# Kernel tuning notes

Measured on AMD Instinct MI355X. Metric: run time of the kernel, lower is better.

## Reference

```python
import jax, jax.numpy as jnp
import numpy as np

HEADS, DIM_HEAD, LANDMARKS, PINV_ITERS = 8, 64, 256, 6
DIM = 512
KERNEL = 33  # residual depthwise conv kernel size (lucidrains NystromAttention default)
EPS = 1e-5   # torch LayerNorm eps


def setup_inputs() -> dict:
    key = jax.random.key(0)
    ks = jax.random.split(key, 4)
    b, n = 4, 8192  # n divisible by LANDMARKS -> no padding branch
    w = lambda k, shape: jax.random.normal(k, shape, dtype=jnp.float32) * 0.02
    return {
        "x": jax.random.normal(ks[0], (b, n, DIM), dtype=jnp.float32),
        "ln_gamma": jnp.ones((DIM,), jnp.float32),
        "ln_beta": jnp.zeros((DIM,), jnp.float32),
        "w_qkv": w(ks[1], (DIM, 3 * HEADS * DIM_HEAD)),   # to_qkv, no bias
        "w_out": w(ks[2], (HEADS * DIM_HEAD, DIM)),
        "b_out": jnp.zeros((DIM,), jnp.float32),
        "res_kernel": w(ks[3], (HEADS, 1, KERNEL, 1)),    # Conv2d(heads, heads, (33,1), groups=heads)
    }


def _moore_penrose_pinv(a, iters):
    # iterative Moore-Penrose pseudoinverse (lucidrains)
    abs_a = jnp.abs(a)
    col = abs_a.sum(-1).max()  # global max, matching torch.max(col)
    row = abs_a.sum(-2).max()
    z = jnp.swapaxes(a, -1, -2) / (col * row)
    I = jnp.eye(a.shape[-1], dtype=a.dtype)
    for _ in range(iters):
        az = a @ z
        z = 0.25 * z @ (13.0 * I - az @ (15.0 * I - az @ (7.0 * I - az)))
    return z


def reference(x, ln_gamma, ln_beta, w_qkv, w_out, b_out, res_kernel):
    b, n, d = x.shape
    h, dh, m = HEADS, DIM_HEAD, LANDMARKS
    # --- LayerNorm ---
    mu = x.mean(-1, keepdims=True)
    var = ((x - mu) ** 2).mean(-1, keepdims=True)
    xn = (x - mu) * jax.lax.rsqrt(var + EPS) * ln_gamma + ln_beta
    # --- qkv projection ---
    qkv = xn @ w_qkv                                   # (b, n, 3*h*dh)
    q, k, v = jnp.split(qkv, 3, axis=-1)
    to_heads = lambda t: t.reshape(b, n, h, dh).transpose(0, 2, 1, 3)  # (b, h, n, dh)
    q, k, v = to_heads(q), to_heads(k), to_heads(v)
    q = q * (dh ** -0.5)
    # --- landmark pooling (mean over groups of l tokens) ---
    l = n // m
    q_l = q.reshape(b, h, m, l, dh).mean(3)            # (b, h, m, dh)
    k_l = k.reshape(b, h, m, l, dh).mean(3)
    # --- three similarity matrices + softmaxes ---
    attn1 = jax.nn.softmax(jnp.einsum('bhnd,bhmd->bhnm', q, k_l), axis=-1)    # (b,h,n,m)
    attn2 = jax.nn.softmax(jnp.einsum('bhid,bhjd->bhij', q_l, k_l), axis=-1)  # (b,h,m,m)
    attn3 = jax.nn.softmax(jnp.einsum('bhmd,bhnd->bhmn', q_l, k), axis=-1)    # (b,h,m,n)
    out = (attn1 @ _moore_penrose_pinv(attn2, PINV_ITERS)) @ (attn3 @ v)      # (b,h,n,dh)
    # --- depthwise residual conv over sequence dim (groups = heads) ---
    res = jax.lax.conv_general_dilated(
        v, res_kernel, window_strides=(1, 1),
        padding=((KERNEL // 2, KERNEL // 2), (0, 0)),
        dimension_numbers=('NCHW', 'OIHW', 'NCHW'),
        feature_group_count=h)
    out = out + res
    # --- merge heads, output projection, outer residual ---
    out = out.transpose(0, 2, 1, 3).reshape(b, n, h * dh)
    att = out @ w_out + b_out
    return x + att
```

## Files before the change

### kernel.cpp

```cpp
#include <hip/hip_runtime.h>
#include <math.h>

#define NB 4
#define NSEQ 8192
#define DMODEL 512
#define NHEADS 8
#define DHEAD 64
#define NLM 256
#define LTOK 32
#define NBH 32
#define KCONV 33
#define CH3 8

typedef unsigned short bf16_t;
typedef __attribute__((ext_vector_type(8))) short bf16x8;
typedef __attribute__((ext_vector_type(4))) float f32x4;

__device__ __forceinline__ float bf2f(bf16_t u) {
  return __uint_as_float(((unsigned)u) << 16);
}
__device__ __forceinline__ bf16_t f2bf(float f) {
  unsigned u = __float_as_uint(f);
  return (bf16_t)((u + 0x7fffu + ((u >> 16) & 1u)) >> 16);
}
__device__ __forceinline__ void bfpair(unsigned u, float& lo, float& hi) {
  lo = __uint_as_float(u << 16);
  hi = __uint_as_float(u & 0xffff0000u);
}
__device__ __forceinline__ void gload16(const bf16_t* g, bf16_t* l) {
  __builtin_amdgcn_global_load_lds(
      (const __attribute__((address_space(1))) unsigned int*)g,
      (__attribute__((address_space(3))) unsigned int*)l, 16, 0, 0);
}

__global__ __launch_bounds__(256) void ln_kernel(const float* __restrict__ x,
    const float* __restrict__ gamma, const float* __restrict__ beta,
    bf16_t* __restrict__ xn) {
  int row = blockIdx.x * 4 + (threadIdx.x >> 6);
  int lane = threadIdx.x & 63;
  const float4* xr = reinterpret_cast<const float4*>(x + (size_t)row * DMODEL);
  float4 a0 = xr[lane];
  float4 a1 = xr[lane + 64];
  float s  = a0.x + a0.y + a0.z + a0.w + a1.x + a1.y + a1.z + a1.w;
  float s2 = a0.x*a0.x + a0.y*a0.y + a0.z*a0.z + a0.w*a0.w
           + a1.x*a1.x + a1.y*a1.y + a1.z*a1.z + a1.w*a1.w;
  #pragma unroll
  for (int off = 32; off; off >>= 1) {
    s  += __shfl_down(s, off);
    s2 += __shfl_down(s2, off);
  }
  s = __shfl(s, 0); s2 = __shfl(s2, 0);
  float mu = s * (1.0f / DMODEL);
  float var = s2 * (1.0f / DMODEL) - mu * mu;
  float rs = rsqrtf(var + 1e-5f);
  const float4* g4 = reinterpret_cast<const float4*>(gamma);
  const float4* b4 = reinterpret_cast<const float4*>(beta);
  float4 g0 = g4[lane], g1 = g4[lane + 64];
  float4 bb0 = b4[lane], bb1 = b4[lane + 64];
  ushort4 o0, o1;
  o0.x = f2bf((a0.x - mu) * rs * g0.x + bb0.x);
  o0.y = f2bf((a0.y - mu) * rs * g0.y + bb0.y);
  o0.z = f2bf((a0.z - mu) * rs * g0.z + bb0.z);
  o0.w = f2bf((a0.w - mu) * rs * g0.w + bb0.w);
  o1.x = f2bf((a1.x - mu) * rs * g1.x + bb1.x);
  o1.y = f2bf((a1.y - mu) * rs * g1.y + bb1.y);
  o1.z = f2bf((a1.z - mu) * rs * g1.z + bb1.z);
  o1.w = f2bf((a1.w - mu) * rs * g1.w + bb1.w);
  ushort4* o = reinterpret_cast<ushort4*>(xn + (size_t)row * DMODEL);
  o[lane] = o0; o[lane + 64] = o1;
}

__global__ void castT2_kernel(const float* __restrict__ wqkv, const float* __restrict__ wout,
                              bf16_t* __restrict__ wqkvT, bf16_t* __restrict__ woutT,
                              unsigned int* __restrict__ scal) {
  int idx = blockIdx.x * 256 + threadIdx.x;
  if (idx == 0) scal[0] = 0x3f800000u;
  if (idx == 1) scal[1] = 0u;
  if (idx < 786432) {
    int k = idx & 511, c = idx >> 9;
    float v = wqkv[(size_t)k * 1536 + c];
    if (c < 512) v *= 0.125f;
    wqkvT[idx] = f2bf(v);
  } else {
    int i = idx - 786432;
    int k = i & 511, c = i >> 9;
    woutT[i] = f2bf(wout[(size_t)k * 512 + c]);
  }
}

__global__ __launch_bounds__(256) void gemm_qkv_mfma(const bf16_t* __restrict__ A,
    const bf16_t* __restrict__ Bt, bf16_t* __restrict__ q, bf16_t* __restrict__ k,
    bf16_t* __restrict__ v) {
  __shared__ __align__(16) bf16_t As0[128 * 32];
  __shared__ __align__(16) bf16_t As1[128 * 32];
  __shared__ __align__(16) bf16_t Bs0[128 * 32];
  __shared__ __align__(16) bf16_t Bs1[128 * 32];
  int bid = blockIdx.x;
  int xcd = bid & 7;
  int idx = bid >> 3;
  int rowT = xcd * 32 + idx / 12;
  int colT = idx % 12;
  int rowB = rowT * 128, colB = colT * 128;
  int tid = threadIdx.x;
  int wave = tid >> 6, lane = tid & 63;
  int wr = (wave >> 1) * 64, wc = (wave & 1) * 64;
  int lrow = lane & 15, g = lane >> 4;
  f32x4 acc[4][4] = {};
  for (int k0 = 0; k0 < DMODEL; k0 += 64) {
    #pragma unroll
    for (int c = 0; c < 2; ++c) {
      int eb = wave * 1024 + c * 512;
      int e = eb + lane * 8;
      int r = e >> 5, cc = e & 31;
      gload16(A + (size_t)(rowB + r) * DMODEL + k0 + cc, &As0[eb]);
      gload16(A + (size_t)(rowB + r) * DMODEL + k0 + 32 + cc, &As1[eb]);
      gload16(Bt + (size_t)(colB + r) * DMODEL + k0 + cc, &Bs0[eb]);
      gload16(Bt + (size_t)(colB + r) * DMODEL + k0 + 32 + cc, &Bs1[eb]);
    }
    __syncthreads();
    #pragma unroll
    for (int ks = 0; ks < 2; ++ks) {
      const bf16_t* Ab2 = ks ? As1 : As0;
      const bf16_t* Bb2 = ks ? Bs1 : Bs0;
      bf16x8 af[4], bf[4];
      #pragma unroll
      for (int m = 0; m < 4; ++m)
        af[m] = *reinterpret_cast<const bf16x8*>(&Ab2[(wr + m * 16 + lrow) * 32 + g * 8]);
      #pragma unroll
      for (int n = 0; n < 4; ++n)
        bf[n] = *reinterpret_cast<const bf16x8*>(&Bb2[(wc + n * 16 + lrow) * 32 + g * 8]);
      #pragma unroll
      for (int m = 0; m < 4; ++m)
        #pragma unroll
        for (int n = 0; n < 4; ++n)
          acc[m][n] = __builtin_amdgcn_mfma_f32_16x16x32_bf16(af[m], bf[n], acc[m][n], 0, 0, 0);
    }
    __syncthreads();
  }
  #pragma unroll
  for (int m = 0; m < 4; ++m) {
    #pragma unroll
    for (int n = 0; n < 4; ++n) {
      int col = colB + wc + n * 16 + lrow;
      int which = col >> 9, hc = col & 511, h = hc >> 6, d = hc & 63;
      bf16_t* dst = (which == 0) ? q : (which == 1 ? k : v);
      #pragma unroll
      for (int r = 0; r < 4; ++r) {
        int row = rowB + wr + m * 16 + g * 4 + r;
        int b = row >> 13, nn = row & 8191;
        dst[((size_t)(b * NHEADS + h) * NSEQ + nn) * DHEAD + d] = f2bf(acc[m][n][r]);
      }
    }
  }
}

__global__ __launch_bounds__(256) void gemm_out_mfma(const bf16_t* __restrict__ A,
    const bf16_t* __restrict__ Bt, const float* __restrict__ bo,
    const float* __restrict__ x, float* __restrict__ y) {
  __shared__ __align__(16) bf16_t As[128 * 32];
  __shared__ __align__(16) bf16_t Bs[128 * 32];
  int rowB = blockIdx.x * 128, colB = blockIdx.y * 128;
  int tid = threadIdx.x;
  int wave = tid >> 6, lane = tid & 63;
  int wr = (wave >> 1) * 64, wc = (wave & 1) * 64;
  int lrow = lane & 15, g = lane >> 4;
  f32x4 acc[4][4] = {};
  for (int k0 = 0; k0 < DMODEL; k0 += 32) {
    #pragma unroll
    for (int c = 0; c < 2; ++c) {
      int eb = wave * 1024 + c * 512;
      int e = eb + lane * 8;
      int r = e >> 5, cc = e & 31;
      gload16(A + (size_t)(rowB + r) * DMODEL + k0 + cc, &As[eb]);
      gload16(Bt + (size_t)(colB + r) * DMODEL + k0 + cc, &Bs[eb]);
    }
    __syncthreads();
    bf16x8 af[4], bf[4];
    #pragma unroll
    for (int m = 0; m < 4; ++m)
      af[m] = *reinterpret_cast<const bf16x8*>(&As[(wr + m * 16 + lrow) * 32 + g * 8]);
    #pragma unroll
    for (int n = 0; n < 4; ++n)
      bf[n] = *reinterpret_cast<const bf16x8*>(&Bs[(wc + n * 16 + lrow) * 32 + g * 8]);
    #pragma unroll
    for (int n = 0; n < 4; ++n)
      #pragma unroll
      for (int m = 0; m < 4; ++m)
        acc[n][m] = __builtin_amdgcn_mfma_f32_16x16x32_bf16(bf[n], af[m], acc[n][m], 0, 0, 0);
    __syncthreads();
  }
  #pragma unroll
  for (int n = 0; n < 4; ++n) {
    int c0 = colB + wc + n * 16 + g * 4;
    float4 b4 = *reinterpret_cast<const float4*>(&bo[c0]);
    #pragma unroll
    for (int m = 0; m < 4; ++m) {
      int row = rowB + wr + m * 16 + lrow;
      size_t off = (size_t)row * DMODEL + c0;
      float4 xv = *reinterpret_cast<const float4*>(&x[off]);
      float4 o;
      o.x = xv.x + b4.x + acc[n][m][0];
      o.y = xv.y + b4.y + acc[n][m][1];
      o.z = xv.z + b4.z + acc[n][m][2];
      o.w = xv.w + b4.w + acc[n][m][3];
      *reinterpret_cast<float4*>(&y[off]) = o;
    }
  }
}

__global__ __launch_bounds__(256) void transpose64_kernel(const bf16_t* __restrict__ src,
    bf16_t* __restrict__ dst, int R) {
  __shared__ __align__(16) bf16_t T[64 * 64];
  int r0 = blockIdx.x * 64, bh = blockIdx.y;
  int tid = threadIdx.x;
  int jj = tid >> 2, part = tid & 3;
  const uint4* sr = reinterpret_cast<const uint4*>(
      src + ((size_t)bh * R + r0 + jj) * 64 + part * 16);
  uint4 a0 = sr[0], a1 = sr[1];
  int xr = (jj >> 3) & 7;
  int pg0 = (part * 2) ^ xr, pg1 = (part * 2 + 1) ^ xr;
  *reinterpret_cast<uint4*>(&T[jj * 64 + pg0 * 8]) = a0;
  *reinterpret_cast<uint4*>(&T[jj * 64 + pg1 * 8]) = a1;
  __syncthreads();
  int d = tid >> 2;
  unsigned ow[8];
  #pragma unroll
  for (int ee = 0; ee < 8; ++ee) {
    int n1 = part * 16 + ee * 2, n2 = n1 + 1;
    unsigned lo = T[n1 * 64 + (((d >> 3) ^ ((n1 >> 3) & 7)) * 8) + (d & 7)];
    unsigned hi = T[n2 * 64 + (((d >> 3) ^ ((n2 >> 3) & 7)) * 8) + (d & 7)];
    ow[ee] = lo | (hi << 16);
  }
  uint4* ot = reinterpret_cast<uint4*>(dst + ((size_t)bh * 64 + d) * R + r0 + part * 16);
  ot[0] = make_uint4(ow[0], ow[1], ow[2], ow[3]);
  ot[1] = make_uint4(ow[4], ow[5], ow[6], ow[7]);
}

__global__ void pool_kernel(const bf16_t* __restrict__ q, const bf16_t* __restrict__ k,
                            float* __restrict__ ql, float* __restrict__ kl,
                            bf16_t* __restrict__ qlb, bf16_t* __restrict__ klb) {
  int idx = blockIdx.x * 256 + threadIdx.x;
  const int half = NBH * NLM * DHEAD;
  const bf16_t* src = (idx < half) ? q : k;
  float* dst = (idx < half) ? ql : kl;
  bf16_t* dstb = (idx < half) ? qlb : klb;
  int i = (idx < half) ? idx : idx - half;
  int d = i & 63, m = (i >> 6) & 255, bh = i >> 14;
  const bf16_t* p = src + ((size_t)bh * NSEQ + m * LTOK) * DHEAD + d;
  float sum = 0.f;
  #pragma unroll
  for (int t = 0; t < LTOK; ++t) sum += bf2f(p[(size_t)t * DHEAD]);
  float r = sum * (1.0f / LTOK);
  dst[i] = r;
  dstb[i] = f2bf(r);
}

__global__ __launch_bounds__(256) void attn2_kernel(const float* __restrict__ ql,
    const float* __restrict__ kl, float* __restrict__ a2) {
  __shared__ float qs[64];
  __shared__ float red[256];
  int bh = blockIdx.y, i = blockIdx.x, t = threadIdx.x;
  if (t < 64) qs[t] = ql[((size_t)bh * NLM + i) * DHEAD + t];
  __syncthreads();
  const float* kr = kl + ((size_t)bh * NLM + t) * DHEAD;
  float s = 0.f;
  #pragma unroll
  for (int d = 0; d < 64; ++d) s += qs[d] * kr[d];
  red[t] = s; __syncthreads();
  for (int off = 128; off; off >>= 1) { if (t < off) red[t] = fmaxf(red[t], red[t + off]); __syncthreads(); }
  float mx = red[0]; __syncthreads();
  float p = expf(s - mx);
  red[t] = p; __syncthreads();
  for (int off = 128; off; off >>= 1) { if (t < off) red[t] += red[t + off]; __syncthreads(); }
  a2[((size_t)bh * NLM + i) * NLM + t] = p / red[0];
}

__global__ void colrow_kernel(const float* __restrict__ a2, unsigned int* __restrict__ scal) {
  int bh = blockIdx.x;
  int t = threadIdx.x;
  const float* Ab = a2 + (size_t)bh * NLM * NLM;
  float sum = 0.f;
  for (int i2 = 0; i2 < NLM; ++i2) sum += fabsf(Ab[(size_t)i2 * NLM + t]);
  __shared__ float red[256];
  red[t] = sum; __syncthreads();
  for (int off = 128; off; off >>= 1) { if (t < off) red[t] = fmaxf(red[t], red[t + off]); __syncthreads(); }
  if (t == 0) atomicMax(&scal[1], __float_as_uint(red[0]));
}

__global__ void zinit_kernel(const float* __restrict__ a2, const unsigned int* __restrict__ scal,
                             bf16_t* __restrict__ zb, bf16_t* __restrict__ a2b) {
  int idx = blockIdx.x * 256 + threadIdx.x;
  float inv = 1.0f / (__uint_as_float(scal[0]) * __uint_as_float(scal[1]));
  int j = idx & 255, i = (idx >> 8) & 255, bh = idx >> 16;
  zb[idx] = f2bf(a2[((size_t)bh * NLM + j) * NLM + i] * inv);
  a2b[idx] = f2bf(a2[idx]);
}

__global__ __launch_bounds__(256) void matmul256_b2b(bf16_t* __restrict__ C,
    const bf16_t* __restrict__ A, const bf16_t* __restrict__ Bm, float s, float alpha) {
  __shared__ __align__(16) bf16_t Ah[64][72];
  __shared__ __align__(16) bf16_t Bh[64][72];
  int bh = blockIdx.y;
  const bf16_t* Ab = A + (size_t)bh * NLM * NLM;
  const bf16_t* Bb = Bm + (size_t)bh * NLM * NLM;
  bf16_t* Cb = C + (size_t)bh * NLM * NLM;
  int rowB = (blockIdx.x >> 2) * 64, colB = (blockIdx.x & 3) * 64;
  int tid = threadIdx.x, w = tid >> 6, lane = tid & 63, tx = lane & 15, g = lane >> 4;
  int jj = tid >> 2, part = tid & 3;
  f32x4 acc[4] = {};
  for (int k0 = 0; k0 < NLM; k0 += 64) {
    {
      const uint4* ar = reinterpret_cast<const uint4*>(
          Ab + (size_t)(rowB + jj) * NLM + k0 + part * 16);
      *reinterpret_cast<uint4*>(&Ah[jj][part * 16]) = ar[0];
      *reinterpret_cast<uint4*>(&Ah[jj][part * 16 + 8]) = ar[1];
      const uint4* br = reinterpret_cast<const uint4*>(
          Bb + (size_t)(k0 + jj) * NLM + colB + part * 16);
      uint4 b0 = br[0], b1 = br[1];
      int d0 = part * 16;
      Bh[d0+ 0][jj] = (bf16_t)(b0.x & 0xffffu); Bh[d0+ 1][jj] = (bf16_t)(b0.x >> 16);
      Bh[d0+ 2][jj] = (bf16_t)(b0.y & 0xffffu); Bh[d0+ 3][jj] = (bf16_t)(b0.y >> 16);
      Bh[d0+ 4][jj] = (bf16_t)(b0.z & 0xffffu); Bh[d0+ 5][jj] = (bf16_t)(b0.z >> 16);
      Bh[d0+ 6][jj] = (bf16_t)(b0.w & 0xffffu); Bh[d0+ 7][jj] = (bf16_t)(b0.w >> 16);
      Bh[d0+ 8][jj] = (bf16_t)(b1.x & 0xffffu); Bh[d0+ 9][jj] = (bf16_t)(b1.x >> 16);
      Bh[d0+10][jj] = (bf16_t)(b1.y & 0xffffu); Bh[d0+11][jj] = (bf16_t)(b1.y >> 16);
      Bh[d0+12][jj] = (bf16_t)(b1.z & 0xffffu); Bh[d0+13][jj] = (bf16_t)(b1.z >> 16);
      Bh[d0+14][jj] = (bf16_t)(b1.w & 0xffffu); Bh[d0+15][jj] = (bf16_t)(b1.w >> 16);
    }
    __syncthreads();
    #pragma unroll
    for (int ks = 0; ks < 2; ++ks) {
      bf16x8 ah = *reinterpret_cast<const bf16x8*>(&Ah[w * 16 + tx][g * 8 + 32 * ks]);
      #pragma unroll
      for (int tn = 0; tn < 4; ++tn) {
        bf16x8 bhf = *reinterpret_cast<const bf16x8*>(&Bh[tn * 16 + tx][g * 8 + 32 * ks]);
        acc[tn] = __builtin_amdgcn_mfma_f32_16x16x32_bf16(bhf, ah, acc[tn], 0, 0, 0);
      }
    }
    __syncthreads();
  }
  int rr = rowB + w * 16 + tx;
  #pragma unroll
  for (int tn = 0; tn < 4; ++tn) {
    int c0 = colB + tn * 16 + g * 4;
    size_t off = (size_t)rr * NLM + c0;
    float a0 = 0.f, a1 = 0.f, a2v = 0.f, a3 = 0.f;
    if (s != 0.0f) {
      ushort4 av = *reinterpret_cast<const ushort4*>(&Ab[off]);
      a0 = bf2f(av.x); a1 = bf2f(av.y); a2v = bf2f(av.z); a3 = bf2f(av.w);
    }
    ushort4 o;
    o.x = f2bf(alpha * (s * a0 - acc[tn][0]));
    o.y = f2bf(alpha * (s * a1 - acc[tn][1]));
    o.z = f2bf(alpha * (s * a2v - acc[tn][2]));
    o.w = f2bf(alpha * (s * a3 - acc[tn][3]));
    *reinterpret_cast<ushort4*>(&Cb[off]) = o;
  }
}

__global__ __launch_bounds__(256) void matmul256_b2b2(
    bf16_t* __restrict__ C0, const bf16_t* __restrict__ A0,
    bf16_t* __restrict__ C1, const bf16_t* __restrict__ A1,
    const bf16_t* __restrict__ Bm, float s, float alpha) {
  __shared__ __align__(16) bf16_t Ah[64][72];
  __shared__ __align__(16) bf16_t Bh[64][72];
  int bh = blockIdx.y;
  const bf16_t* A = (blockIdx.z == 0) ? A0 : A1;
  bf16_t* C = (blockIdx.z == 0) ? C0 : C1;
  const bf16_t* Ab = A + (size_t)bh * NLM * NLM;
  const bf16_t* Bb = Bm + (size_t)bh * NLM * NLM;
  bf16_t* Cb = C + (size_t)bh * NLM * NLM;
  int rowB = (blockIdx.x >> 2) * 64, colB = (blockIdx.x & 3) * 64;
  int tid = threadIdx.x, w = tid >> 6, lane = tid & 63, tx = lane & 15, g = lane >> 4;
  int jj = tid >> 2, part = tid & 3;
  f32x4 acc[4] = {};
  for (int k0 = 0; k0 < NLM; k0 += 64) {
    {
      const uint4* ar = reinterpret_cast<const uint4*>(
          Ab + (size_t)(rowB + jj) * NLM + k0 + part * 16);
      *reinterpret_cast<uint4*>(&Ah[jj][part * 16]) = ar[0];
      *reinterpret_cast<uint4*>(&Ah[jj][part * 16 + 8]) = ar[1];
      const uint4* br = reinterpret_cast<const uint4*>(
          Bb + (size_t)(k0 + jj) * NLM + colB + part * 16);
      uint4 b0 = br[0], b1 = br[1];
      int d0 = part * 16;
      Bh[d0+ 0][jj] = (bf16_t)(b0.x & 0xffffu); Bh[d0+ 1][jj] = (bf16_t)(b0.x >> 16);
      Bh[d0+ 2][jj] = (bf16_t)(b0.y & 0xffffu); Bh[d0+ 3][jj] = (bf16_t)(b0.y >> 16);
      Bh[d0+ 4][jj] = (bf16_t)(b0.z & 0xffffu); Bh[d0+ 5][jj] = (bf16_t)(b0.z >> 16);
      Bh[d0+ 6][jj] = (bf16_t)(b0.w & 0xffffu); Bh[d0+ 7][jj] = (bf16_t)(b0.w >> 16);
      Bh[d0+ 8][jj] = (bf16_t)(b1.x & 0xffffu); Bh[d0+ 9][jj] = (bf16_t)(b1.x >> 16);
      Bh[d0+10][jj] = (bf16_t)(b1.y & 0xffffu); Bh[d0+11][jj] = (bf16_t)(b1.y >> 16);
      Bh[d0+12][jj] = (bf16_t)(b1.z & 0xffffu); Bh[d0+13][jj] = (bf16_t)(b1.z >> 16);
      Bh[d0+14][jj] = (bf16_t)(b1.w & 0xffffu); Bh[d0+15][jj] = (bf16_t)(b1.w >> 16);
    }
    __syncthreads();
    #pragma unroll
    for (int ks = 0; ks < 2; ++ks) {
      bf16x8 ah = *reinterpret_cast<const bf16x8*>(&Ah[w * 16 + tx][g * 8 + 32 * ks]);
      #pragma unroll
      for (int tn = 0; tn < 4; ++tn) {
        bf16x8 bhf = *reinterpret_cast<const bf16x8*>(&Bh[tn * 16 + tx][g * 8 + 32 * ks]);
        acc[tn] = __builtin_amdgcn_mfma_f32_16x16x32_bf16(bhf, ah, acc[tn], 0, 0, 0);
      }
    }
    __syncthreads();
  }
  int rr = rowB + w * 16 + tx;
  #pragma unroll
  for (int tn = 0; tn < 4; ++tn) {
    int c0 = colB + tn * 16 + g * 4;
    size_t off = (size_t)rr * NLM + c0;
    ushort4 av = *reinterpret_cast<const ushort4*>(&Ab[off]);
    float a0 = bf2f(av.x), a1 = bf2f(av.y), a2v = bf2f(av.z), a3 = bf2f(av.w);
    ushort4 o;
    o.x = f2bf(alpha * (s * a0 - acc[tn][0]));
    o.y = f2bf(alpha * (s * a1 - acc[tn][1]));
    o.z = f2bf(alpha * (s * a2v - acc[tn][2]));
    o.w = f2bf(alpha * (s * a3 - acc[tn][3]));
    *reinterpret_cast<ushort4*>(&Cb[off]) = o;
  }
}

__global__ __launch_bounds__(256) void matmul256_b2f(float* __restrict__ C,
    const bf16_t* __restrict__ A, const bf16_t* __restrict__ Bm, float s, float alpha) {
  __shared__ __align__(16) bf16_t Ah[64][72];
  __shared__ __align__(16) bf16_t Bh[64][72];
  int bh = blockIdx.y;
  const bf16_t* Ab = A + (size_t)bh * NLM * NLM;
  const bf16_t* Bb = Bm + (size_t)bh * NLM * NLM;
  float* Cb = C + (size_t)bh * NLM * NLM;
  int rowB = (blockIdx.x >> 2) * 64, colB = (blockIdx.x & 3) * 64;
  int tid = threadIdx.x, w = tid >> 6, lane = tid & 63, tx = lane & 15, g = lane >> 4;
  int jj = tid >> 2, part = tid & 3;
  f32x4 acc[4] = {};
  for (int k0 = 0; k0 < NLM; k0 += 64) {
    {
      const uint4* ar = reinterpret_cast<const uint4*>(
          Ab + (size_t)(rowB + jj) * NLM + k0 + part * 16);
      *reinterpret_cast<uint4*>(&Ah[jj][part * 16]) = ar[0];
      *reinterpret_cast<uint4*>(&Ah[jj][part * 16 + 8]) = ar[1];
      const uint4* br = reinterpret_cast<const uint4*>(
          Bb + (size_t)(k0 + jj) * NLM + colB + part * 16);
      uint4 b0 = br[0], b1 = br[1];
      int d0 = part * 16;
      Bh[d0+ 0][jj] = (bf16_t)(b0.x & 0xffffu); Bh[d0+ 1][jj] = (bf16_t)(b0.x >> 16);
      Bh[d0+ 2][jj] = (bf16_t)(b0.y & 0xffffu); Bh[d0+ 3][jj] = (bf16_t)(b0.y >> 16);
      Bh[d0+ 4][jj] = (bf16_t)(b0.z & 0xffffu); Bh[d0+ 5][jj] = (bf16_t)(b0.z >> 16);
      Bh[d0+ 6][jj] = (bf16_t)(b0.w & 0xffffu); Bh[d0+ 7][jj] = (bf16_t)(b0.w >> 16);
      Bh[d0+ 8][jj] = (bf16_t)(b1.x & 0xffffu); Bh[d0+ 9][jj] = (bf16_t)(b1.x >> 16);
      Bh[d0+10][jj] = (bf16_t)(b1.y & 0xffffu); Bh[d0+11][jj] = (bf16_t)(b1.y >> 16);
      Bh[d0+12][jj] = (bf16_t)(b1.z & 0xffffu); Bh[d0+13][jj] = (bf16_t)(b1.z >> 16);
      Bh[d0+14][jj] = (bf16_t)(b1.w & 0xffffu); Bh[d0+15][jj] = (bf16_t)(b1.w >> 16);
    }
    __syncthreads();
    #pragma unroll
    for (int ks = 0; ks < 2; ++ks) {
      bf16x8 ah = *reinterpret_cast<const bf16x8*>(&Ah[w * 16 + tx][g * 8 + 32 * ks]);
      #pragma unroll
      for (int tn = 0; tn < 4; ++tn) {
        bf16x8 bhf = *reinterpret_cast<const bf16x8*>(&Bh[tn * 16 + tx][g * 8 + 32 * ks]);
        acc[tn] = __builtin_amdgcn_mfma_f32_16x16x32_bf16(bhf, ah, acc[tn], 0, 0, 0);
      }
    }
    __syncthreads();
  }
  int rr = rowB + w * 16 + tx;
  #pragma unroll
  for (int tn = 0; tn < 4; ++tn) {
    int c0 = colB + tn * 16 + g * 4;
    size_t off = (size_t)rr * NLM + c0;
    float a0 = 0.f, a1 = 0.f, a2v = 0.f, a3 = 0.f;
    if (s != 0.0f) {
      ushort4 av = *reinterpret_cast<const ushort4*>(&Ab[off]);
      a0 = bf2f(av.x); a1 = bf2f(av.y); a2v = bf2f(av.z); a3 = bf2f(av.w);
    }
    float4 o;
    o.x = alpha * (s * a0 - acc[tn][0]);
    o.y = alpha * (s * a1 - acc[tn][1]);
    o.z = alpha * (s * a2v - acc[tn][2]);
    o.w = alpha * (s * a3 - acc[tn][3]);
    *reinterpret_cast<float4*>(&Cb[off]) = o;
  }
}

__global__ __launch_bounds__(256) void attn3v_mfma(const bf16_t* __restrict__ qlb,
    const bf16_t* __restrict__ k, const bf16_t* __restrict__ vT,
    float* __restrict__ Wpart, float* __restrict__ mlpart) {
  __shared__ __align__(16) bf16_t Qs0[2048], Qs1[2048];
  __shared__ __align__(16) bf16_t Ks0[2048], Ks1[2048];
  __shared__ __align__(16) bf16_t Vs0[2048], Vs1[2048];
  __shared__ __align__(16) bf16_t Ps[64][72];
  int chunk = blockIdx.x, lmt = blockIdx.y, bh = blockIdx.z;
  int tid = threadIdx.x;
  int wave = tid >> 6, lane = tid & 63;
  int w = wave, tx = lane & 15, g = lane >> 4;
  int lm0 = lmt * 64;
  const bf16_t* kb = k + (size_t)bh * NSEQ * DHEAD;
  const bf16_t* vtb = vT + (size_t)bh * DHEAD * NSEQ;
  int eb = wave * 512;
  int e = eb + lane * 8;
  int sr = e >> 5, sc = e & 31;
  {
    const bf16_t* qrow = qlb + ((size_t)bh * NLM + lm0 + sr) * DHEAD;
    gload16(qrow + sc, &Qs0[eb]);
    gload16(qrow + 32 + sc, &Qs1[eb]);
  }
  f32x4 oacc[4] = {};
  float lreg[4] = {0.f, 0.f, 0.f, 0.f};
  __syncthreads();
  bf16x8 aq0 = *reinterpret_cast<const bf16x8*>(&Qs0[(w * 16 + tx) * 32 + g * 8]);
  bf16x8 aq1 = *reinterpret_cast<const bf16x8*>(&Qs1[(w * 16 + tx) * 32 + g * 8]);
  for (int it = 0; it < NSEQ / (CH3 * 64); ++it) {
    int n0 = chunk * (NSEQ / CH3) + it * 64;
    {
      const bf16_t* krow = kb + (size_t)(n0 + sr) * DHEAD;
      gload16(krow + sc, &Ks0[eb]);
      gload16(krow + 32 + sc, &Ks1[eb]);
      const bf16_t* vrow = vtb + (size_t)sr * NSEQ + n0;
      gload16(vrow + sc, &Vs0[eb]);
      gload16(vrow + 32 + sc, &Vs1[eb]);
    }
    __syncthreads();
    f32x4 sacc[4] = {};
    #pragma unroll
    for (int tn = 0; tn < 4; ++tn) {
      bf16x8 bk0 = *reinterpret_cast<const bf16x8*>(&Ks0[(tn * 16 + tx) * 32 + g * 8]);
      bf16x8 bk1 = *reinterpret_cast<const bf16x8*>(&Ks1[(tn * 16 + tx) * 32 + g * 8]);
      sacc[tn] = __builtin_amdgcn_mfma_f32_16x16x32_bf16(aq0, bk0, sacc[tn], 0, 0, 0);
      sacc[tn] = __builtin_amdgcn_mfma_f32_16x16x32_bf16(aq1, bk1, sacc[tn], 0, 0, 0);
    }
    #pragma unroll
    for (int r = 0; r < 4; ++r) {
      float p0 = __expf(sacc[0][r]);
      float p1 = __expf(sacc[1][r]);
      float p2 = __expf(sacc[2][r]);
      float p3 = __expf(sacc[3][r]);
      float ts = p0 + p1 + p2 + p3;
      #pragma unroll
      for (int off = 1; off < 16; off <<= 1) ts += __shfl_xor(ts, off);
      lreg[r] += ts;
      int prow = w * 16 + g * 4 + r;
      Ps[prow][tx]      = f2bf(p0);
      Ps[prow][tx + 16] = f2bf(p1);
      Ps[prow][tx + 32] = f2bf(p2);
      Ps[prow][tx + 48] = f2bf(p3);
    }
    __syncthreads();
    bf16x8 ap0 = *reinterpret_cast<const bf16x8*>(&Ps[w * 16 + tx][g * 8]);
    bf16x8 ap1 = *reinterpret_cast<const bf16x8*>(&Ps[w * 16 + tx][g * 8 + 32]);
    #pragma unroll
    for (int td = 0; td < 4; ++td) {
      bf16x8 bv0 = *reinterpret_cast<const bf16x8*>(&Vs0[(td * 16 + tx) * 32 + g * 8]);
      bf16x8 bv1 = *reinterpret_cast<const bf16x8*>(&Vs1[(td * 16 + tx) * 32 + g * 8]);
      oacc[td] = __builtin_amdgcn_mfma_f32_16x16x32_bf16(bv0, ap0, oacc[td], 0, 0, 0);
      oacc[td] = __builtin_amdgcn_mfma_f32_16x16x32_bf16(bv1, ap1, oacc[td], 0, 0, 0);
    }
    __syncthreads();
  }
  size_t ob = ((size_t)(chunk * NBH + bh) * NLM + lm0 + w * 16 + tx);
  #pragma unroll
  for (int td = 0; td < 4; ++td) {
    float4 w4 = make_float4(oacc[td][0], oacc[td][1], oacc[td][2], oacc[td][3]);
    *reinterpret_cast<float4*>(&Wpart[ob * DHEAD + td * 16 + g * 4]) = w4;
  }
  if (tx == 0) {
    #pragma unroll
    for (int r = 0; r < 4; ++r) {
      size_t obr = ((size_t)(chunk * NBH + bh) * NLM + lm0 + w * 16 + g * 4 + r);
      mlpart[obr] = lreg[r];
    }
  }
}

__global__ void attn3v_combine(const float* __restrict__ Wpart,
    const float* __restrict__ mlpart, float* __restrict__ Wm) {
  int idx = blockIdx.x * 256 + threadIdx.x;
  int d = idx & 63;
  int s0 = idx >> 6;
  const int CHS = NBH * NLM;
  float L = 0.f, wv = 0.f;
  #pragma unroll
  for (int c = 0; c < CH3; ++c) {
    L += mlpart[(size_t)c * CHS + s0];
    wv += Wpart[((size_t)c * CHS + s0) * DHEAD + d];
  }
  Wm[idx] = wv / L;
}

__global__ void zw_kernel(const float* __restrict__ z, const float* __restrict__ W,
                          bf16_t* __restrict__ Ub) {
  int idx = blockIdx.x * 256 + threadIdx.x;
  int d = idx & 63, i = (idx >> 6) & 255, bh = idx >> 14;
  const float* zr = z + ((size_t)bh * NLM + i) * NLM;
  const float* Wb = W + (size_t)bh * NLM * DHEAD + d;
  float acc = 0.f;
  for (int j = 0; j < NLM; ++j) acc += zr[j] * Wb[(size_t)j * DHEAD];
  Ub[idx] = f2bf(acc);
}

__global__ __launch_bounds__(256) void attn1_mfma(const bf16_t* __restrict__ q,
    const bf16_t* __restrict__ klb, const bf16_t* __restrict__ Ut,
    bf16_t* __restrict__ outp) {
  __shared__ __align__(16) bf16_t Qs0[2048], Qs1[2048];
  __shared__ __align__(16) bf16_t Ks0[2048], Ks1[2048];
  __shared__ __align__(16) bf16_t Vs0[2048], Vs1[2048];
  __shared__ __align__(16) bf16_t Ps[64][72];
  int nt = blockIdx.x, bh = blockIdx.y;
  int tid = threadIdx.x;
  int wave = tid >> 6, lane = tid & 63;
  int w = wave, tx = lane & 15, g = lane >> 4;
  int n0 = nt * 64;
  int b = bh >> 3, h = bh & 7;
  const bf16_t* klbb = klb + (size_t)bh * NLM * DHEAD;
  const bf16_t* utb = Ut + (size_t)bh * DHEAD * NLM;
  int eb = wave * 512;
  int e = eb + lane * 8;
  int sr = e >> 5, sc = e & 31;
  {
    const bf16_t* qrow = q + ((size_t)bh * NSEQ + n0 + sr) * DHEAD;
    gload16(qrow + sc, &Qs0[eb]);
    gload16(qrow + 32 + sc, &Qs1[eb]);
  }
  f32x4 oacc[4] = {};
  float lreg[4] = {0.f, 0.f, 0.f, 0.f};
  __syncthreads();
  bf16x8 aq0 = *reinterpret_cast<const bf16x8*>(&Qs0[(w * 16 + tx) * 32 + g * 8]);
  bf16x8 aq1 = *reinterpret_cast<const bf16x8*>(&Qs1[(w * 16 + tx) * 32 + g * 8]);
  for (int it = 0; it < 4; ++it) {
    int lm0 = it * 64;
    {
      const bf16_t* krow = klbb + (size_t)(lm0 + sr) * DHEAD;
      gload16(krow + sc, &Ks0[eb]);
      gload16(krow + 32 + sc, &Ks1[eb]);
      const bf16_t* urow = utb + (size_t)sr * NLM + lm0;
      gload16(urow + sc, &Vs0[eb]);
      gload16(urow + 32 + sc, &Vs1[eb]);
    }
    __syncthreads();
    f32x4 sacc[4] = {};
    #pragma unroll
    for (int tn = 0; tn < 4; ++tn) {
      bf16x8 bk0 = *reinterpret_cast<const bf16x8*>(&Ks0[(tn * 16 + tx) * 32 + g * 8]);
      bf16x8 bk1 = *reinterpret_cast<const bf16x8*>(&Ks1[(tn * 16 + tx) * 32 + g * 8]);
      sacc[tn] = __builtin_amdgcn_mfma_f32_16x16x32_bf16(aq0, bk0, sacc[tn], 0, 0, 0);
      sacc[tn] = __builtin_amdgcn_mfma_f32_16x16x32_bf16(aq1, bk1, sacc[tn], 0, 0, 0);
    }
    #pragma unroll
    for (int r = 0; r < 4; ++r) {
      float p0 = __expf(sacc[0][r]);
      float p1 = __expf(sacc[1][r]);
      float p2 = __expf(sacc[2][r]);
      float p3 = __expf(sacc[3][r]);
      float ts = p0 + p1 + p2 + p3;
      #pragma unroll
      for (int off = 1; off < 16; off <<= 1) ts += __shfl_xor(ts, off);
      lreg[r] += ts;
      int prow = w * 16 + g * 4 + r;
      Ps[prow][tx]      = f2bf(p0);
      Ps[prow][tx + 16] = f2bf(p1);
      Ps[prow][tx + 32] = f2bf(p2);
      Ps[prow][tx + 48] = f2bf(p3);
    }
    __syncthreads();
    bf16x8 ap0 = *reinterpret_cast<const bf16x8*>(&Ps[w * 16 + tx][g * 8]);
    bf16x8 ap1 = *reinterpret_cast<const bf16x8*>(&Ps[w * 16 + tx][g * 8 + 32]);
    #pragma unroll
    for (int td = 0; td < 4; ++td) {
      bf16x8 bv0 = *reinterpret_cast<const bf16x8*>(&Vs0[(td * 16 + tx) * 32 + g * 8]);
      bf16x8 bv1 = *reinterpret_cast<const bf16x8*>(&Vs1[(td * 16 + tx) * 32 + g * 8]);
      oacc[td] = __builtin_amdgcn_mfma_f32_16x16x32_bf16(bv0, ap0, oacc[td], 0, 0, 0);
      oacc[td] = __builtin_amdgcn_mfma_f32_16x16x32_bf16(bv1, ap1, oacc[td], 0, 0, 0);
    }
    __syncthreads();
  }
  float sel = lreg[0];
  sel = ((tx & 3) == 1) ? lreg[1] : sel;
  sel = ((tx & 3) == 2) ? lreg[2] : sel;
  sel = ((tx & 3) == 3) ? lreg[3] : sel;
  float inv = 1.0f / __shfl(sel, ((tx >> 2) << 4) | (tx & 3));
  int n = n0 + w * 16 + tx;
  #pragma unroll
  for (int td = 0; td < 4; ++td) {
    ushort4 o;
    o.x = f2bf(oacc[td][0] * inv);
    o.y = f2bf(oacc[td][1] * inv);
    o.z = f2bf(oacc[td][2] * inv);
    o.w = f2bf(oacc[td][3] * inv);
    *reinterpret_cast<ushort4*>(
        &outp[((size_t)(b * NSEQ + n)) * DMODEL + h * DHEAD + td * 16 + g * 4]) = o;
  }
}

__global__ __launch_bounds__(256) void conv_kernel(const bf16_t* __restrict__ vT,
    const float* __restrict__ rk, bf16_t* __restrict__ outp) {
  int tile = blockIdx.x, bh = blockIdx.y;
  int b = bh >> 3, h = bh & 7;
  int tid = threadIdx.x;
  int w = tid >> 6, d = tid & 63;
  const bf16_t* vrow = vT + ((size_t)bh * DHEAD + d) * NSEQ;
  const float* wk = rk + h * KCONV;
  int nbase = tile * 256 + w * 64;
  for (int i = 0; i < 8; ++i) {
    int ns = nbase + i * 8;
    int lo = ns - 16;
    __attribute__((aligned(16))) unsigned wv[20];
    if (lo >= 0 && ns + 24 <= NSEQ) {
      #pragma unroll
      for (int u = 0; u < 5; ++u)
        *reinterpret_cast<uint4*>(&wv[u * 4]) =
            *reinterpret_cast<const uint4*>(vrow + lo + u * 8);
    } else {
      #pragma unroll
      for (int u = 0; u < 20; ++u) {
        int n0e = lo + u * 2, n1e = n0e + 1;
        unsigned l16 = (n0e >= 0 && n0e < NSEQ) ? (unsigned)vrow[n0e] : 0u;
        unsigned h16 = (n1e >= 0 && n1e < NSEQ) ? (unsigned)vrow[n1e] : 0u;
        wv[u] = l16 | (h16 << 16);
      }
    }
    #pragma unroll
    for (int j = 0; j < 8; ++j) {
      float acc = 0.f;
      #pragma unroll
      for (int t = 0; t < KCONV; ++t) {
        int ix = j + t;
        unsigned word = wv[ix >> 1];
        float xv = __uint_as_float((ix & 1) ? (word & 0xffff0000u) : (word << 16));
        acc += wk[t] * xv;
      }
      int n = ns + j;
      size_t ob = ((size_t)(b * NSEQ + n)) * DMODEL + h * DHEAD + d;
      outp[ob] = f2bf(bf2f(outp[ob]) + acc);
    }
  }
}

extern "C" void kernel_launch(void* const* d_in, const int* in_sizes, int n_in,
                              void* d_out, int out_size, void* d_ws, size_t ws_size,
                              hipStream_t stream) {
  const float* x     = (const float*)d_in[0];
  const float* gamma = (const float*)d_in[1];
  const float* beta  = (const float*)d_in[2];
  const float* wqkv  = (const float*)d_in[3];
  const float* wout  = (const float*)d_in[4];
  const float* bout  = (const float*)d_in[5];
  const float* rk    = (const float*)d_in[6];
  float* y = (float*)d_out;

  char* wsb = (char*)d_ws;
  bf16_t* xn = (bf16_t*)(wsb);
  bf16_t* q  = (bf16_t*)(wsb + 33554432ull);
  bf16_t* k  = (bf16_t*)(wsb + 67108864ull);
  bf16_t* v  = (bf16_t*)(wsb + 100663296ull);
  float* a2f = (float*)(wsb + 134217728ull);
  bf16_t* M2b = (bf16_t*)(wsb + 134217728ull);
  bf16_t* M3b = (bf16_t*)(wsb + 138412032ull);
  bf16_t* a2b = (bf16_t*)(wsb + 150994944ull);
  bf16_t* zA  = (bf16_t*)(wsb + 155189248ull);
  bf16_t* zB  = (bf16_t*)(wsb + 159383552ull);
  bf16_t* YA  = (bf16_t*)(wsb + 163577856ull);
  bf16_t* YB  = (bf16_t*)(wsb + 167772160ull);
  float* zf  = (float*)(wsb + 150994944ull);
  float* ql  = (float*)(wsb + 176160768ull);
  float* kl  = (float*)(wsb + 178257920ull);
  float* Wm  = (float*)(wsb + 180355072ull);
  bf16_t* Ub = (bf16_t*)(wsb + 182452224ull);
  unsigned int* scal = (unsigned int*)(wsb + 184549376ull);
  bf16_t* wqkvT = (bf16_t*)(wsb + 182452224ull);
  bf16_t* woutT = (bf16_t*)(wsb + 184549440ull);
  bf16_t* qlb = (bf16_t*)(wsb + 185073728ull);
  bf16_t* klb = (bf16_t*)(wsb + 186122304ull);
  bf16_t* Ut  = (bf16_t*)(wsb + 187170880ull);

  bf16_t* vT = xn;
  float* Wpart  = (float*)(wsb + 134217728ull);
  float* mlpart = (float*)(wsb + 167772160ull);
  bf16_t* out_pre = (bf16_t*)(wsb + 134217728ull);

  castT2_kernel<<<4096, 256, 0, stream>>>(wqkv, wout, wqkvT, woutT, scal);
  ln_kernel<<<8192, 256, 0, stream>>>(x, gamma, beta, xn);
  gemm_qkv_mfma<<<3072, 256, 0, stream>>>(xn, wqkvT, q, k, v);
  transpose64_kernel<<<dim3(128, 32), 256, 0, stream>>>(v, vT, NSEQ);
  pool_kernel<<<4096, 256, 0, stream>>>(q, k, ql, kl, qlb, klb);
  attn2_kernel<<<dim3(256, 32), 256, 0, stream>>>(ql, kl, a2f);
  colrow_kernel<<<32, 256, 0, stream>>>(a2f, scal);
  zinit_kernel<<<8192, 256, 0, stream>>>(a2f, scal, zA, a2b);

  matmul256_b2b<<<dim3(16, 32), 256, 0, stream>>>(YA, a2b, zA, 0.f, -1.f);
  bf16_t *zc = zA, *zn = zB, *Yc = YA, *Yn = YB;
  for (int it = 0; it < 5; ++it) {
    matmul256_b2b<<<dim3(16, 32), 256, 0, stream>>>(M2b, Yc, Yc, 7.f, 1.f);
    matmul256_b2b<<<dim3(16, 32), 256, 0, stream>>>(M3b, Yc, M2b, 15.f, 1.f);
    matmul256_b2b2<<<dim3(16, 32, 2), 256, 0, stream>>>(zn, zc, Yn, Yc, M3b, 13.f, 0.25f);
    bf16_t* t;
    t = zc; zc = zn; zn = t;
    t = Yc; Yc = Yn; Yn = t;
  }
  matmul256_b2b<<<dim3(16, 32), 256, 0, stream>>>(M2b, Yc, Yc, 7.f, 1.f);
  matmul256_b2b<<<dim3(16, 32), 256, 0, stream>>>(M3b, Yc, M2b, 15.f, 1.f);
  matmul256_b2f<<<dim3(16, 32), 256, 0, stream>>>(zf, zc, M3b, 13.f, 0.25f);

  attn3v_mfma<<<dim3(CH3, 4, 32), 256, 0, stream>>>(qlb, k, vT, Wpart, mlpart);
  attn3v_combine<<<2048, 256, 0, stream>>>(Wpart, mlpart, Wm);
  zw_kernel<<<2048, 256, 0, stream>>>(zf, Wm, Ub);
  transpose64_kernel<<<dim3(4, 32), 256, 0, stream>>>(Ub, Ut, NLM);
  attn1_mfma<<<dim3(128, 32), 256, 0, stream>>>(q, klb, Ut, out_pre);
  conv_kernel<<<dim3(32, 32), 256, 0, stream>>>(vT, rk, out_pre);
  gemm_out_mfma<<<dim3(256, 4), 256, 0, stream>>>(out_pre, woutT, bout, x, y);
}
```

Before: 601.5 us.

## Restructure pinv iteration to two batched matmul launches per step

The Newton-Schulz pinv step is rewritten algebraically: it first computes P = Y·Y and N = z·Y together in one batched launch, then computes the next Y and z from (7Y − P) in a second launch, folding the 13/15 constant terms into the epilogue. This cuts three dependent kernel launches per iteration to two and removes one serial matmul stage from the chain. The cost is an extra elementwise combine while staging B tiles, plus a different bf16 rounding order that can shift numerical error in the pseudoinverse.

```diff
diff --git a/kernel.cpp b/kernel.cpp
--- a/kernel.cpp
+++ b/kernel.cpp
@@ -26,6 +26,11 @@
 __device__ __forceinline__ void bfpair(unsigned u, float& lo, float& hi) {
   lo = __uint_as_float(u << 16);
   hi = __uint_as_float(u & 0xffff0000u);
+}
+__device__ __forceinline__ bf16_t comb7(unsigned yw, unsigned pw, bool hi) {
+  float yv = __uint_as_float(hi ? (yw & 0xffff0000u) : (yw << 16));
+  float pv = __uint_as_float(hi ? (pw & 0xffff0000u) : (pw << 16));
+  return f2bf(7.0f * yv - pv);
 }
 __device__ __forceinline__ void gload16(const bf16_t* g, bf16_t* l) {
   __builtin_amdgcn_global_load_lds(
@@ -410,8 +415,11 @@
   for (int tn = 0; tn < 4; ++tn) {
     int c0 = colB + tn * 16 + g * 4;
     size_t off = (size_t)rr * NLM + c0;
-    ushort4 av = *reinterpret_cast<const ushort4*>(&Ab[off]);
-    float a0 = bf2f(av.x), a1 = bf2f(av.y), a2v = bf2f(av.z), a3 = bf2f(av.w);
+    float a0 = 0.f, a1 = 0.f, a2v = 0.f, a3 = 0.f;
+    if (s != 0.0f) {
+      ushort4 av = *reinterpret_cast<const ushort4*>(&Ab[off]);
+      a0 = bf2f(av.x); a1 = bf2f(av.y); a2v = bf2f(av.z); a3 = bf2f(av.w);
+    }
     ushort4 o;
     o.x = f2bf(alpha * (s * a0 - acc[tn][0]));
     o.y = f2bf(alpha * (s * a1 - acc[tn][1]));
@@ -421,13 +429,84 @@
   }
 }
 
-__global__ __launch_bounds__(256) void matmul256_b2f(float* __restrict__ C,
-    const bf16_t* __restrict__ A, const bf16_t* __restrict__ Bm, float s, float alpha) {
+__global__ __launch_bounds__(256) void matmul256_b2b2m3(
+    bf16_t* __restrict__ C0, const bf16_t* __restrict__ A0, const bf16_t* __restrict__ E0,
+    bf16_t* __restrict__ C1, const bf16_t* __restrict__ A1, const bf16_t* __restrict__ E1,
+    const bf16_t* __restrict__ Ym, const bf16_t* __restrict__ Pm) {
+  __shared__ __align__(16) bf16_t Ah[64][72];
+  __shared__ __align__(16) bf16_t Bh[64][72];
+  int bh = blockIdx.y;
+  const bf16_t* A = (blockIdx.z == 0) ? A0 : A1;
+  const bf16_t* E = (blockIdx.z == 0) ? E0 : E1;
+  bf16_t* C = (blockIdx.z == 0) ? C0 : C1;
+  const bf16_t* Ab = A + (size_t)bh * NLM * NLM;
+  const bf16_t* Eb = E + (size_t)bh * NLM * NLM;
+  const bf16_t* Yb = Ym + (size_t)bh * NLM * NLM;
+  const bf16_t* Pb = Pm + (size_t)bh * NLM * NLM;
+  bf16_t* Cb = C + (size_t)bh * NLM * NLM;
+  int rowB = (blockIdx.x >> 2) * 64, colB = (blockIdx.x & 3) * 64;
+  int tid = threadIdx.x, w = tid >> 6, lane = tid & 63, tx = lane & 15, g = lane >> 4;
+  int jj = tid >> 2, part = tid & 3;
+  f32x4 acc[4] = {};
+  for (int k0 = 0; k0 < NLM; k0 += 64) {
+    {
+      const uint4* ar = reinterpret_cast<const uint4*>(
+          Ab + (size_t)(rowB + jj) * NLM + k0 + part * 16);
+      *reinterpret_cast<uint4*>(&Ah[jj][part * 16]) = ar[0];
+      *reinterpret_cast<uint4*>(&Ah[jj][part * 16 + 8]) = ar[1];
+      size_t boff = (size_t)(k0 + jj) * NLM + colB + part * 16;
+      const uint4* yr = reinterpret_cast<const uint4*>(Yb + boff);
+      const uint4* pr = reinterpret_cast<const uint4*>(Pb + boff);
+      uint4 y0 = yr[0], y1 = yr[1];
+      uint4 p0 = pr[0], p1 = pr[1];
+      int d0 = part * 16;
+      Bh[d0+ 0][jj] = comb7(y0.x, p0.x, false); Bh[d0+ 1][jj] = comb7(y0.x, p0.x, true);
+      Bh[d0+ 2][jj] = comb7(y0.y, p0.y, false); Bh[d0+ 3][jj] = comb7(y0.y, p0.y, true);
+      Bh[d0+ 4][jj] = comb7(y0.z, p0.z, false); Bh[d0+ 5][jj] = comb7(y0.z, p0.z, true);
+      Bh[d0+ 6][jj] = comb7(y0.w, p0.w, false); Bh[d0+ 7][jj] = comb7(y0.w, p0.w, true);
+      Bh[d0+ 8][jj] = comb7(y1.x, p1.x, false); Bh[d0+ 9][jj] = comb7(y1.x, p1.x, true);
+      Bh[d0+10][jj] = comb7(y1.y, p1.y, false); Bh[d0+11][jj] = comb7(y1.y, p1.y, true);
+      Bh[d0+12][jj] = comb7(y1.z, p1.z, false); Bh[d0+13][jj] = comb7(y1.z, p1.z, true);
+      Bh[d0+14][jj] = comb7(y1.w, p1.w, false); Bh[d0+15][jj] = comb7(y1.w, p1.w, true);
+    }
+    __syncthreads();
+    #pragma unroll
+    for (int ks = 0; ks < 2; ++ks) {
+      bf16x8 ah = *reinterpret_cast<const bf16x8*>(&Ah[w * 16 + tx][g * 8 + 32 * ks]);
+      #pragma unroll
+      for (int tn = 0; tn < 4; ++tn) {
+        bf16x8 bhf = *reinterpret_cast<const bf16x8*>(&Bh[tn * 16 + tx][g * 8 + 32 * ks]);
+        acc[tn] = __builtin_amdgcn_mfma_f32_16x16x32_bf16(bhf, ah, acc[tn], 0, 0, 0);
+      }
+    }
+    __syncthreads();
+  }
+  int rr = rowB + w * 16 + tx;
+  #pragma unroll
+  for (int tn = 0; tn < 4; ++tn) {
+    int c0 = colB + tn * 16 + g * 4;
+    size_t off = (size_t)rr * NLM + c0;
+    ushort4 av = *reinterpret_cast<const ushort4*>(&Ab[off]);
+    ushort4 ev = *reinterpret_cast<const ushort4*>(&Eb[off]);
+    ushort4 o;
+    o.x = f2bf(0.25f * (13.f * bf2f(ev.x) - 15.f * bf2f(av.x) + acc[tn][0]));
+    o.y = f2bf(0.25f * (13.f * bf2f(ev.y) - 15.f * bf2f(av.y) + acc[tn][1]));
+    o.z = f2bf(0.25f * (13.f * bf2f(ev.z) - 15.f * bf2f(av.z) + acc[tn][2]));
+    o.w = f2bf(0.25f * (13.f * bf2f(ev.w) - 15.f * bf2f(av.w) + acc[tn][3]));
+    *reinterpret_cast<ushort4*>(&Cb[off]) = o;
+  }
+}
+
+__global__ __launch_bounds__(256) void matmul256_b2fm3(float* __restrict__ C,
+    const bf16_t* __restrict__ A, const bf16_t* __restrict__ E,
+    const bf16_t* __restrict__ Ym, const bf16_t* __restrict__ Pm) {
   __shared__ __align__(16) bf16_t Ah[64][72];
   __shared__ __align__(16) bf16_t Bh[64][72];
   int bh = blockIdx.y;
   const bf16_t* Ab = A + (size_t)bh * NLM * NLM;
-  const bf16_t* Bb = Bm + (size_t)bh * NLM * NLM;
+  const bf16_t* Eb = E + (size_t)bh * NLM * NLM;
+  const bf16_t* Yb = Ym + (size_t)bh * NLM * NLM;
+  const bf16_t* Pb = Pm + (size_t)bh * NLM * NLM;
   float* Cb = C + (size_t)bh * NLM * NLM;
   int rowB = (blockIdx.x >> 2) * 64, colB = (blockIdx.x & 3) * 64;
   int tid = threadIdx.x, w = tid >> 6, lane = tid & 63, tx = lane & 15, g = lane >> 4;
@@ -439,18 +518,20 @@
           Ab + (size_t)(rowB + jj) * NLM + k0 + part * 16);
       *reinterpret_cast<uint4*>(&Ah[jj][part * 16]) = ar[0];
       *reinterpret_cast<uint4*>(&Ah[jj][part * 16 + 8]) = ar[1];
-      const uint4* br = reinterpret_cast<const uint4*>(
-          Bb + (size_t)(k0 + jj) * NLM + colB + part * 16);
-      uint4 b0 = br[0], b1 = br[1];
+      size_t boff = (size_t)(k0 + jj) * NLM + colB + part * 16;
+      const uint4* yr = reinterpret_cast<const uint4*>(Yb + boff);
+      const uint4* pr = reinterpret_cast<const uint4*>(Pb + boff);
+      uint4 y0 = yr[0], y1 = yr[1];
+      uint4 p0 = pr[0], p1 = pr[1];
       int d0 = part * 16;
-      Bh[d0+ 0][jj] = (bf16_t)(b0.x & 0xffffu); Bh[d0+ 1][jj] = (bf16_t)(b0.x >> 16);
-      Bh[d0+ 2][jj] = (bf16_t)(b0.y & 0xffffu); Bh[d0+ 3][jj] = (bf16_t)(b0.y >> 16);
-      Bh[d0+ 4][jj] = (bf16_t)(b0.z & 0xffffu); Bh[d0+ 5][jj] = (bf16_t)(b0.z >> 16);
-      Bh[d0+ 6][jj] = (bf16_t)(b0.w & 0xffffu); Bh[d0+ 7][jj] = (bf16_t)(b0.w >> 16);
-      Bh[d0+ 8][jj] = (bf16_t)(b1.x & 0xffffu); Bh[d0+ 9][jj] = (bf16_t)(b1.x >> 16);
-      Bh[d0+10][jj] = (bf16_t)(b1.y & 0xffffu); Bh[d0+11][jj] = (bf16_t)(b1.y >> 16);
-      Bh[d0+12][jj] = (bf16_t)(b1.z & 0xffffu); Bh[d0+13][jj] = (bf16_t)(b1.z >> 16);
-      Bh[d0+14][jj] = (bf16_t)(b1.w & 0xffffu); Bh[d0+15][jj] = (bf16_t)(b1.w >> 16);
+      Bh[d0+ 0][jj] = comb7(y0.x, p0.x, false); Bh[d0+ 1][jj] = comb7(y0.x, p0.x, true);
+      Bh[d0+ 2][jj] = comb7(y0.y, p0.y, false); Bh[d0+ 3][jj] = comb7(y0.y, p0.y, true);
+      Bh[d0+ 4][jj] = comb7(y0.z, p0.z, false); Bh[d0+ 5][jj] = comb7(y0.z, p0.z, true);
+      Bh[d0+ 6][jj] = comb7(y0.w, p0.w, false); Bh[d0+ 7][jj] = comb7(y0.w, p0.w, true);
+      Bh[d0+ 8][jj] = comb7(y1.x, p1.x, false); Bh[d0+ 9][jj] = comb7(y1.x, p1.x, true);
+      Bh[d0+10][jj] = comb7(y1.y, p1.y, false); Bh[d0+11][jj] = comb7(y1.y, p1.y, true);
+      Bh[d0+12][jj] = comb7(y1.z, p1.z, false); Bh[d0+13][jj] = comb7(y1.z, p1.z, true);
+      Bh[d0+14][jj] = comb7(y1.w, p1.w, false); Bh[d0+15][jj] = comb7(y1.w, p1.w, true);
     }
     __syncthreads();
     #pragma unroll
@@ -469,16 +550,13 @@
   for (int tn = 0; tn < 4; ++tn) {
     int c0 = colB + tn * 16 + g * 4;
     size_t off = (size_t)rr * NLM + c0;
-    float a0 = 0.f, a1 = 0.f, a2v = 0.f, a3 = 0.f;
-    if (s != 0.0f) {
-      ushort4 av = *reinterpret_cast<const ushort4*>(&Ab[off]);
-      a0 = bf2f(av.x); a1 = bf2f(av.y); a2v = bf2f(av.z); a3 = bf2f(av.w);
-    }
+    ushort4 av = *reinterpret_cast<const ushort4*>(&Ab[off]);
+    ushort4 ev = *reinterpret_cast<const ushort4*>(&Eb[off]);
     float4 o;
-    o.x = alpha * (s * a0 - acc[tn][0]);
-    o.y = alpha * (s * a1 - acc[tn][1]);
-    o.z = alpha * (s * a2v - acc[tn][2]);
-    o.w = alpha * (s * a3 - acc[tn][3]);
+    o.x = 0.25f * (13.f * bf2f(ev.x) - 15.f * bf2f(av.x) + acc[tn][0]);
+    o.y = 0.25f * (13.f * bf2f(ev.y) - 15.f * bf2f(av.y) + acc[tn][1]);
+    o.z = 0.25f * (13.f * bf2f(ev.z) - 15.f * bf2f(av.z) + acc[tn][2]);
+    o.w = 0.25f * (13.f * bf2f(ev.w) - 15.f * bf2f(av.w) + acc[tn][3]);
     *reinterpret_cast<float4*>(&Cb[off]) = o;
   }
 }
@@ -753,8 +831,8 @@
   bf16_t* k  = (bf16_t*)(wsb + 67108864ull);
   bf16_t* v  = (bf16_t*)(wsb + 100663296ull);
   float* a2f = (float*)(wsb + 134217728ull);
-  bf16_t* M2b = (bf16_t*)(wsb + 134217728ull);
-  bf16_t* M3b = (bf16_t*)(wsb + 138412032ull);
+  bf16_t* Pb = (bf16_t*)(wsb + 134217728ull);
+  bf16_t* Nb = (bf16_t*)(wsb + 138412032ull);
   bf16_t* a2b = (bf16_t*)(wsb + 150994944ull);
   bf16_t* zA  = (bf16_t*)(wsb + 155189248ull);
   bf16_t* zB  = (bf16_t*)(wsb + 159383552ull);
@@ -789,16 +867,14 @@
   matmul256_b2b<<<dim3(16, 32), 256, 0, stream>>>(YA, a2b, zA, 0.f, -1.f);
   bf16_t *zc = zA, *zn = zB, *Yc = YA, *Yn = YB;
   for (int it = 0; it < 5; ++it) {
-    matmul256_b2b<<<dim3(16, 32), 256, 0, stream>>>(M2b, Yc, Yc, 7.f, 1.f);
-    matmul256_b2b<<<dim3(16, 32), 256, 0, stream>>>(M3b, Yc, M2b, 15.f, 1.f);
-    matmul256_b2b2<<<dim3(16, 32, 2), 256, 0, stream>>>(zn, zc, Yn, Yc, M3b, 13.f, 0.25f);
+    matmul256_b2b2<<<dim3(16, 32, 2), 256, 0, stream>>>(Pb, Yc, Nb, zc, Yc, 0.f, -1.f);
+    matmul256_b2b2m3<<<dim3(16, 32, 2), 256, 0, stream>>>(Yn, Pb, Yc, zn, Nb, zc, Yc, Pb);
     bf16_t* t;
     t = zc; zc = zn; zn = t;
     t = Yc; Yc = Yn; Yn = t;
   }
-  matmul256_b2b<<<dim3(16, 32), 256, 0, stream>>>(M2b, Yc, Yc, 7.f, 1.f);
-  matmul256_b2b<<<dim3(16, 32), 256, 0, stream>>>(M3b, Yc, M2b, 15.f, 1.f);
-  matmul256_b2f<<<dim3(16, 32), 256, 0, stream>>>(zf, zc, M3b, 13.f, 0.25f);
+  matmul256_b2b2<<<dim3(16, 32, 2), 256, 0, stream>>>(Pb, Yc, Nb, zc, Yc, 0.f, -1.f);
+  matmul256_b2fm3<<<dim3(16, 32), 256, 0, stream>>>(zf, Nb, zc, Yc, Pb);
 
   attn3v_mfma<<<dim3(CH3, 4, 32), 256, 0, stream>>>(qlb, k, vT, Wpart, mlpart);
   attn3v_combine<<<2048, 256, 0, stream>>>(Wpart, mlpart, Wm);
```

Measured after the change: 599.9 us. About the same (-0.3%).
